# Performance work log

Measured on AMD Instinct MI355X. Metric: run time of the kernel, lower is better.

## Reference

```python
import jax, jax.numpy as jnp
import numpy as np

DIM = 768
NUM_HEADS = 12
HEAD_DIM = DIM // NUM_HEADS
SCALE = HEAD_DIM ** -0.5


def setup_inputs() -> dict:
    key = jax.random.key(0)
    k1, k2, k3, k4 = jax.random.split(key, 4)
    B, N, C = 4, 2048, DIM
    x = jax.random.normal(k1, (B, N, C), dtype=jnp.float32)
    # nn.Linear(dim, 3*dim, bias=False): weight shape (3C, C), y = x @ W^T
    w_qkv = jax.random.normal(k2, (3 * C, C), dtype=jnp.float32) * (C ** -0.5)
    # nn.Linear(dim, dim) with default bias=True
    w_proj = jax.random.normal(k3, (C, C), dtype=jnp.float32) * (C ** -0.5)
    b_proj = jax.random.normal(k4, (C,), dtype=jnp.float32) * 0.02
    return {"x": x, "w_qkv": w_qkv, "w_proj": w_proj, "b_proj": b_proj}


def reference(x, w_qkv, w_proj, b_proj):
    B, N, C = x.shape
    H, D = NUM_HEADS, HEAD_DIM
    qkv = jnp.einsum('bnc,oc->bno', x, w_qkv)  # (B, N, 3C)
    qkv = qkv.reshape(B, N, 3, H, D).transpose(2, 0, 3, 1, 4)  # (3, B, H, N, D)
    q, k, v = qkv[0], qkv[1], qkv[2]
    attn = jnp.einsum('bhnd,bhmd->bhnm', q, k) * jnp.float32(SCALE)  # (B,H,N,N)
    attn = jax.nn.softmax(attn, axis=-1)
    out = jnp.einsum('bhnm,bhmd->bhnd', attn, v)  # (B,H,N,D)
    out = out.transpose(0, 2, 1, 3).reshape(B, N, C)
    out = jnp.einsum('bnc,oc->bno', out, w_proj) + b_proj
    return out
```

## Files before the change

kernel.cpp:

```cpp
#include <hip/hip_runtime.h>
#include <math.h>

#define B_ 4
#define N_ 2048
#define C_ 768
#define H_ 12
#define D_ 64
#define QKSCALE_ 0.18033688011112042f

typedef unsigned short u16;
typedef unsigned int u32;
typedef short s16x8 __attribute__((ext_vector_type(8)));
typedef float f32x4 __attribute__((ext_vector_type(4)));
typedef float f32x16 __attribute__((ext_vector_type(16)));

__device__ __forceinline__ u16 f2bf(float f) {
    union { float f; u32 u; } v; v.f = f;
    u32 r = (v.u + 0x7fffu + ((v.u >> 16) & 1u)) >> 16;
    return (u16)r;
}

__device__ __forceinline__ void gl_lds16(const u16* g, u16* l) {
    __builtin_amdgcn_global_load_lds(
        (__attribute__((address_space(1))) void*)g,
        (__attribute__((address_space(3))) void*)l, 16, 0, 0);
}

#define NX4_  (B_ * N_ * C_ / 4)
#define NWQ4_ (3 * C_ * C_ / 4)
#define NWP4_ (C_ * C_ / 4)
__global__ __launch_bounds__(256) void cvt_all(const float4* __restrict__ x,
                                               const float4* __restrict__ wq,
                                               const float4* __restrict__ wp,
                                               ushort4* __restrict__ xb,
                                               ushort4* __restrict__ wqb,
                                               ushort4* __restrict__ wpb)
{
    const int tot = NX4_ + NWQ4_ + NWP4_;
    int i = blockIdx.x * blockDim.x + threadIdx.x;
    const int stride = gridDim.x * blockDim.x;
    for (; i < tot; i += stride) {
        const float4* s; ushort4* d; int j;
        if (i < NX4_)              { s = x;  d = xb;  j = i; }
        else if (i < NX4_ + NWQ4_) { s = wq; d = wqb; j = i - NX4_; }
        else                       { s = wp; d = wpb; j = i - NX4_ - NWQ4_; }
        float4 v = s[j];
        ushort4 o;
        o.x = f2bf(v.x); o.y = f2bf(v.y); o.z = f2bf(v.z); o.w = f2bf(v.w);
        d[j] = o;
    }
}

template<int BM, int WPEU, bool OUT_BF16, bool BIAS, bool QSCALE>
__global__ __launch_bounds__(256, WPEU) void gemm_mfma(const u16* __restrict__ A,
                                                       const u16* __restrict__ Bm,
                                                       const float* __restrict__ bias,
                                                       void* __restrict__ Cout,
                                                       int M, int N, int K)
{
    constexpr int MF  = BM / 32;
    constexpr int AC  = BM / 32;
    constexpr int ASZ = BM * 64, BSZ = 128 * 64;
    __shared__ __align__(16) u16 As[2 * ASZ];
    __shared__ __align__(16) u16 Bs[2 * BSZ];
    const int tid  = threadIdx.x;
    const int wv   = tid >> 6;
    const int lane = tid & 63;
    const int lr   = lane & 15;
    const int lq   = lane >> 4;
    const int wm   = (wv >> 1) * (BM / 2);
    const int wn   = (wv & 1) * 64;
    const int row0 = blockIdx.y * BM, col0 = blockIdx.x * 128;

    f32x4 acc[MF][4];
    #pragma unroll
    for (int i = 0; i < MF; i++)
        #pragma unroll
        for (int j = 0; j < 4; j++) { f32x4 z = {0.f,0.f,0.f,0.f}; acc[i][j] = z; }

    const int srow   = lane >> 3;
    const int schunk = ((lane & 7) ^ srow) * 8;

    const int arow_base = (BM / 4) * wv;
    const u16* gA = A + (size_t)(row0 + arow_base + srow) * K + schunk;
    const u16* gB = Bm + (size_t)(col0 + 32 * wv + srow) * K + schunk;
    const int aoff = arow_base * 64;
    const int boff = (32 * wv) * 64;

    const int nIter = K / 64;

    #pragma unroll
    for (int c = 0; c < AC; c++)
        gl_lds16(gA + (size_t)(8 * c) * K, As + aoff + c * 8 * 64);
    #pragma unroll
    for (int c = 0; c < 4; c++)
        gl_lds16(gB + (size_t)(8 * c) * K, Bs + boff + c * 8 * 64);

    for (int t = 0; t < nIter; t++) {
        const int cur = t & 1;
        __syncthreads();
        if (t + 1 < nIter) {
            const int k1 = (t + 1) * 64;
            const int nb = cur ^ 1;
            #pragma unroll
            for (int c = 0; c < AC; c++)
                gl_lds16(gA + (size_t)(8 * c) * K + k1, As + nb * ASZ + aoff + c * 8 * 64);
            #pragma unroll
            for (int c = 0; c < 4; c++)
                gl_lds16(gB + (size_t)(8 * c) * K + k1, Bs + nb * BSZ + boff + c * 8 * 64);
        }
        const u16* __restrict__ Ac = As + cur * ASZ;
        const u16* __restrict__ Bc = Bs + cur * BSZ;
        #pragma unroll
        for (int kk = 0; kk < 2; kk++) {
            const int fo = ((4 * kk + lq) ^ (lr & 7)) * 8;
            s16x8 af[MF], bfr[4];
            #pragma unroll
            for (int i = 0; i < MF; i++)
                af[i] = *(const s16x8*)&Ac[(wm + 16*i + lr) * 64 + fo];
            #pragma unroll
            for (int j = 0; j < 4; j++)
                bfr[j] = *(const s16x8*)&Bc[(wn + 16*j + lr) * 64 + fo];
            #pragma unroll
            for (int i = 0; i < MF; i++)
                #pragma unroll
                for (int j = 0; j < 4; j++)
                    acc[i][j] = __builtin_amdgcn_mfma_f32_16x16x32_bf16(af[i], bfr[j], acc[i][j], 0, 0, 0);
        }
    }

    #pragma unroll
    for (int i = 0; i < MF; i++) {
        #pragma unroll
        for (int j = 0; j < 4; j++) {
            const int col = col0 + wn + 16*j + lr;
            float bv = BIAS ? bias[col] : 0.f;
            #pragma unroll
            for (int r = 0; r < 4; r++) {
                const int row = row0 + wm + 16*i + lq*4 + r;
                float v = acc[i][j][r] + bv;
                if (QSCALE && col < C_) v *= QKSCALE_;
                if (OUT_BF16) ((u16*)Cout)[(size_t)row * N + col] = f2bf(v);
                else          ((float*)Cout)[(size_t)row * N + col] = v;
            }
        }
    }
}

__global__ __launch_bounds__(256, 3) void attn_mfma(const u16* __restrict__ qkv,
                                                    u16* __restrict__ attout)
{
    __shared__ __align__(16) u16 Ks[2][64 * 64];
    __shared__ __align__(16) u16 Vt[2][64][72];

    const int tid  = threadIdx.x;
    const int wv   = tid >> 6;
    const int lane = tid & 63;
    const int l31  = lane & 31;
    const int hi   = lane >> 5;

    const int wgid = blockIdx.y * gridDim.x + blockIdx.x;
    const int ix   = wgid >> 3;
    const int bh   = (wgid & 7) * 6 + (ix >> 4);
    const int n0   = (ix & 15) * 128;
    const int b = bh / H_, h = bh % H_;
    const size_t rs = 3 * C_;

    const u16* Qg = qkv + ((size_t)b * N_ + n0) * rs + h * D_;
    const u16* Kg = qkv + ((size_t)b * N_) * rs + C_ + h * D_;
    const u16* Vg = Kg + C_;

    s16x8 qf[4];
    #pragma unroll
    for (int kk = 0; kk < 4; kk++)
        qf[kk] = *(const s16x8*)(Qg + (size_t)(32*wv + l31) * rs + kk*16 + hi*8);

    const f32x16 z16 = {0.f,0.f,0.f,0.f,0.f,0.f,0.f,0.f,
                        0.f,0.f,0.f,0.f,0.f,0.f,0.f,0.f};
    f32x16 oacc[2] = {z16, z16};
    float li = 0.f;

    const int kkey = lane >> 3;
    const u16* Kg_l = Kg + (size_t)(16*wv + kkey) * rs + ((lane & 7) ^ kkey) * 8;

    const int vc = tid & 7, vp = tid >> 3;
    const int vkey0 = 2 * vp, vd0 = vc * 8;
    const int vcol0 = (vkey0 + 8 * vc) & 63;

    gl_lds16(Kg_l,                    &Ks[0][(16*wv) * 64]);
    gl_lds16(Kg_l + (size_t)8 * rs,   &Ks[0][(16*wv + 8) * 64]);

    s16x8 vr0, vr1;
    {
        const u16* vp2 = Vg + (size_t)vkey0 * rs + vd0;
        vr0 = *(const s16x8*)vp2; vr1 = *(const s16x8*)(vp2 + rs);
    }
    #pragma unroll
    for (int u = 0; u < 8; u++) {
        u32 pk = (u32)(u16)vr0[u] | ((u32)(u16)vr1[u] << 16);
        *(u32*)&Vt[0][vd0 + u][vcol0] = pk;
    }
    {
        const u16* vp2 = Vg + (size_t)(64 + vkey0) * rs + vd0;
        vr0 = *(const s16x8*)vp2; vr1 = *(const s16x8*)(vp2 + rs);
    }

    const int NT = N_ / 64;
    for (int t = 0; t < NT; t++) {
        const int cur = t & 1, nxt = cur ^ 1;
        __syncthreads();
        if (t + 1 < NT) {
            const size_t ko = (size_t)(t + 1) * 64 * rs;
            gl_lds16(Kg_l + ko,                  &Ks[nxt][(16*wv) * 64]);
            gl_lds16(Kg_l + ko + (size_t)8 * rs, &Ks[nxt][(16*wv + 8) * 64]);
            #pragma unroll
            for (int u = 0; u < 8; u++) {
                u32 pk = (u32)(u16)vr0[u] | ((u32)(u16)vr1[u] << 16);
                *(u32*)&Vt[nxt][vd0 + u][vcol0] = pk;
            }
        }
        if (t + 2 < NT) {
            const u16* vp2 = Vg + (size_t)((t+2)*64 + vkey0) * rs + vd0;
            vr0 = *(const s16x8*)vp2; vr1 = *(const s16x8*)(vp2 + rs);
        }

        #define KF(j, kk) (*(const s16x8*)&Ks[cur][(32*(j) + l31) * 64 + \
                           ((2*(kk) + hi) ^ (l31 & 7)) * 8])
        f32x16 st0 = __builtin_amdgcn_mfma_f32_32x32x16_bf16(KF(0,0), qf[0], z16, 0, 0, 0);
        f32x16 st1 = __builtin_amdgcn_mfma_f32_32x32x16_bf16(KF(1,0), qf[0], z16, 0, 0, 0);
        #pragma unroll
        for (int kk = 1; kk < 4; kk++) {
            st0 = __builtin_amdgcn_mfma_f32_32x32x16_bf16(KF(0,kk), qf[kk], st0, 0, 0, 0);
            st1 = __builtin_amdgcn_mfma_f32_32x32x16_bf16(KF(1,kk), qf[kk], st1, 0, 0, 0);
        }
        #undef KF

        #pragma unroll
        for (int j = 0; j < 2; j++) {
            const f32x16 s = j ? st1 : st0;
            float p[16];
            #pragma unroll
            for (int r = 0; r < 16; r++) p[r] = __builtin_amdgcn_exp2f(s[r]);
            #pragma unroll
            for (int r = 0; r < 16; r += 4)
                li += (p[r] + p[r+1]) + (p[r+2] + p[r+3]);
            u32 w[4][2];
            #pragma unroll
            for (int m = 0; m < 4; m++) {
                asm("v_cvt_pk_bf16_f32 %0, %1, %2"
                    : "=v"(w[m][0]) : "v"(p[4*m+0]), "v"(p[4*m+1]));
                asm("v_cvt_pk_bf16_f32 %0, %1, %2"
                    : "=v"(w[m][1]) : "v"(p[4*m+2]), "v"(p[4*m+3]));
            }
            #pragma unroll
            for (int h2 = 0; h2 < 2; h2++) {
                asm("v_permlane32_swap_b32 %0, %1"
                    : "+v"(w[2*h2][0]), "+v"(w[2*h2+1][0]));
                asm("v_permlane32_swap_b32 %0, %1"
                    : "+v"(w[2*h2][1]), "+v"(w[2*h2+1][1]));
                const int sp = 2*j + h2;
                union { u32 uw[4]; s16x8 v; } pa;
                pa.uw[0] = w[2*h2][0];   pa.uw[1] = w[2*h2][1];
                pa.uw[2] = w[2*h2+1][0]; pa.uw[3] = w[2*h2+1][1];
                #pragma unroll
                for (int j2 = 0; j2 < 2; j2++) {
                    const int pb = (2*sp + hi + 4*j2 + (l31 >> 3)) & 7;
                    s16x8 vb = *(const s16x8*)&Vt[cur][32*j2 + l31][pb * 8];
                    oacc[j2] = __builtin_amdgcn_mfma_f32_32x32x16_bf16(pa.v, vb, oacc[j2], 0, 0, 0);
                }
            }
        }
    }

    li += __shfl_xor(li, 32);
    const float inv = 1.f / li;
    #pragma unroll
    for (int r = 0; r < 16; r++) {
        const int qr = (r & 3) + 8 * (r >> 2) + 4 * hi;
        const float iv = __shfl(inv, qr);
        const size_t grow = (size_t)(b * N_ + n0 + 32*wv + qr);
        #pragma unroll
        for (int j2 = 0; j2 < 2; j2++)
            attout[grow * C_ + h * D_ + 32*j2 + l31] = f2bf(oacc[j2][r] * iv);
    }
}

extern "C" void kernel_launch(void* const* d_in, const int* in_sizes, int n_in,
                              void* d_out, int out_size, void* d_ws, size_t ws_size,
                              hipStream_t stream) {
    const float* x      = (const float*)d_in[0];
    const float* w_qkv  = (const float*)d_in[1];
    const float* w_proj = (const float*)d_in[2];
    const float* b_proj = (const float*)d_in[3];
    float* out = (float*)d_out;

    const int NX   = B_ * N_ * C_;
    const int NWQ  = 3 * C_ * C_;
    const int NWP  = C_ * C_;
    const int NQKV = B_ * N_ * 3 * C_;

    u16* xb   = (u16*)d_ws;
    u16* wqb  = xb + NX;
    u16* wpb  = wqb + NWQ;
    u16* qkvb = wpb + NWP;
    u16* attb = qkvb + NQKV;

    dim3 blk(256);

    cvt_all<<<768, blk, 0, stream>>>((const float4*)x, (const float4*)w_qkv,
                                     (const float4*)w_proj,
                                     (ushort4*)xb, (ushort4*)wqb, (ushort4*)wpb);

    const int M = B_ * N_;
    gemm_mfma<128, 2, true, false, true><<<dim3((3*C_)/128, M/128), blk, 0, stream>>>(
        xb, wqb, nullptr, qkvb, M, 3*C_, C_);

    attn_mfma<<<dim3(N_/128, B_ * H_), blk, 0, stream>>>(qkvb, attb);

    gemm_mfma<64, 3, false, true, false><<<dim3(C_/128, M/64), blk, 0, stream>>>(
        attb, wpb, b_proj, out, M, C_, C_);
}
```

Baseline: 212.2 us.

## Process two 32-row query tiles per wave in attention, halving block threads

The attention kernel now runs 2 waves (128 threads) per block instead of 4, and each wave handles 64 query rows as two 32-row tiles. Each K fragment read from LDS and each V fragment feeds two MFMAs instead of one, which halves LDS read traffic per unit of compute. The cooperative K/V staging now has each thread load twice as much. In exchange the kernel needs more registers per wave (two sets of accumulators, Q fragments and softmax sums), and each block has fewer waves to hide latency, which may lower occupancy.

```diff
diff --git a/kernel.cpp b/kernel.cpp
--- a/kernel.cpp
+++ b/kernel.cpp
@@ -147,7 +147,7 @@
     }
 }
 
-__global__ __launch_bounds__(256, 3) void attn_mfma(const u16* __restrict__ qkv,
+__global__ __launch_bounds__(128, 2) void attn_mfma(const u16* __restrict__ qkv,
                                                     u16* __restrict__ attout)
 {
     __shared__ __align__(16) u16 Ks[2][64 * 64];
@@ -170,40 +170,48 @@
     const u16* Kg = qkv + ((size_t)b * N_) * rs + C_ + h * D_;
     const u16* Vg = Kg + C_;
 
-    s16x8 qf[4];
-    #pragma unroll
-    for (int kk = 0; kk < 4; kk++)
-        qf[kk] = *(const s16x8*)(Qg + (size_t)(32*wv + l31) * rs + kk*16 + hi*8);
+    s16x8 qf[2][4];
+    #pragma unroll
+    for (int q = 0; q < 2; q++)
+        #pragma unroll
+        for (int kk = 0; kk < 4; kk++)
+            qf[q][kk] = *(const s16x8*)(Qg + (size_t)(64*wv + 32*q + l31) * rs + kk*16 + hi*8);
 
     const f32x16 z16 = {0.f,0.f,0.f,0.f,0.f,0.f,0.f,0.f,
                         0.f,0.f,0.f,0.f,0.f,0.f,0.f,0.f};
-    f32x16 oacc[2] = {z16, z16};
-    float li = 0.f;
+    f32x16 oacc[2][2] = {{z16, z16}, {z16, z16}};
+    float li[2] = {0.f, 0.f};
 
     const int kkey = lane >> 3;
-    const u16* Kg_l = Kg + (size_t)(16*wv + kkey) * rs + ((lane & 7) ^ kkey) * 8;
+    const u16* Kg_l = Kg + (size_t)(32*wv + kkey) * rs + ((lane & 7) ^ kkey) * 8;
 
     const int vc = tid & 7, vp = tid >> 3;
-    const int vkey0 = 2 * vp, vd0 = vc * 8;
-    const int vcol0 = (vkey0 + 8 * vc) & 63;
-
-    gl_lds16(Kg_l,                    &Ks[0][(16*wv) * 64]);
-    gl_lds16(Kg_l + (size_t)8 * rs,   &Ks[0][(16*wv + 8) * 64]);
-
-    s16x8 vr0, vr1;
-    {
-        const u16* vp2 = Vg + (size_t)vkey0 * rs + vd0;
-        vr0 = *(const s16x8*)vp2; vr1 = *(const s16x8*)(vp2 + rs);
-    }
-    #pragma unroll
-    for (int u = 0; u < 8; u++) {
-        u32 pk = (u32)(u16)vr0[u] | ((u32)(u16)vr1[u] << 16);
-        *(u32*)&Vt[0][vd0 + u][vcol0] = pk;
-    }
-    {
-        const u16* vp2 = Vg + (size_t)(64 + vkey0) * rs + vd0;
-        vr0 = *(const s16x8*)vp2; vr1 = *(const s16x8*)(vp2 + rs);
-    }
+    const int vkey0 = 4 * vp, vd0 = vc * 8;
+    const int col01 = (vkey0     + vd0) & 63;
+    const int col23 = (vkey0 + 2 + vd0) & 63;
+
+    s16x8 vr[4];
+    #define VLOAD(t) do { \
+        const u16* vp2 = Vg + ((size_t)(t)*64 + vkey0) * rs + vd0; \
+        vr[0] = *(const s16x8*)vp2;            vr[1] = *(const s16x8*)(vp2 + rs); \
+        vr[2] = *(const s16x8*)(vp2 + 2*rs);   vr[3] = *(const s16x8*)(vp2 + 3*rs); \
+    } while (0)
+    #define VWRITE(slot) do { \
+        _Pragma("unroll") \
+        for (int u = 0; u < 8; u++) { \
+            u32 pkA = (u32)(u16)vr[0][u] | ((u32)(u16)vr[1][u] << 16); \
+            u32 pkB = (u32)(u16)vr[2][u] | ((u32)(u16)vr[3][u] << 16); \
+            *(u32*)&Vt[slot][vd0 + u][col01] = pkA; \
+            *(u32*)&Vt[slot][vd0 + u][col23] = pkB; \
+        } \
+    } while (0)
+
+    #pragma unroll
+    for (int c = 0; c < 4; c++)
+        gl_lds16(Kg_l + (size_t)(8*c) * rs, &Ks[0][(32*wv + 8*c) * 64]);
+    VLOAD(0);
+    VWRITE(0);
+    VLOAD(1);
 
     const int NT = N_ / 64;
     for (int t = 0; t < NT; t++) {
@@ -211,78 +219,99 @@
         __syncthreads();
         if (t + 1 < NT) {
             const size_t ko = (size_t)(t + 1) * 64 * rs;
-            gl_lds16(Kg_l + ko,                  &Ks[nxt][(16*wv) * 64]);
-            gl_lds16(Kg_l + ko + (size_t)8 * rs, &Ks[nxt][(16*wv + 8) * 64]);
-            #pragma unroll
-            for (int u = 0; u < 8; u++) {
-                u32 pk = (u32)(u16)vr0[u] | ((u32)(u16)vr1[u] << 16);
-                *(u32*)&Vt[nxt][vd0 + u][vcol0] = pk;
-            }
-        }
-        if (t + 2 < NT) {
-            const u16* vp2 = Vg + (size_t)((t+2)*64 + vkey0) * rs + vd0;
-            vr0 = *(const s16x8*)vp2; vr1 = *(const s16x8*)(vp2 + rs);
-        }
+            #pragma unroll
+            for (int c = 0; c < 4; c++)
+                gl_lds16(Kg_l + ko + (size_t)(8*c) * rs, &Ks[nxt][(32*wv + 8*c) * 64]);
+            VWRITE(nxt);
+        }
+        if (t + 2 < NT)
+            VLOAD(t + 2);
 
         #define KF(j, kk) (*(const s16x8*)&Ks[cur][(32*(j) + l31) * 64 + \
                            ((2*(kk) + hi) ^ (l31 & 7)) * 8])
-        f32x16 st0 = __builtin_amdgcn_mfma_f32_32x32x16_bf16(KF(0,0), qf[0], z16, 0, 0, 0);
-        f32x16 st1 = __builtin_amdgcn_mfma_f32_32x32x16_bf16(KF(1,0), qf[0], z16, 0, 0, 0);
-        #pragma unroll
-        for (int kk = 1; kk < 4; kk++) {
-            st0 = __builtin_amdgcn_mfma_f32_32x32x16_bf16(KF(0,kk), qf[kk], st0, 0, 0, 0);
-            st1 = __builtin_amdgcn_mfma_f32_32x32x16_bf16(KF(1,kk), qf[kk], st1, 0, 0, 0);
-        }
+        f32x16 st[2][2];
+        #pragma unroll
+        for (int j = 0; j < 2; j++) {
+            s16x8 kf = KF(j, 0);
+            st[0][j] = __builtin_amdgcn_mfma_f32_32x32x16_bf16(kf, qf[0][0], z16, 0, 0, 0);
+            st[1][j] = __builtin_amdgcn_mfma_f32_32x32x16_bf16(kf, qf[1][0], z16, 0, 0, 0);
+        }
+        #pragma unroll
+        for (int kk = 1; kk < 4; kk++)
+            #pragma unroll
+            for (int j = 0; j < 2; j++) {
+                s16x8 kf = KF(j, kk);
+                st[0][j] = __builtin_amdgcn_mfma_f32_32x32x16_bf16(kf, qf[0][kk], st[0][j], 0, 0, 0);
+                st[1][j] = __builtin_amdgcn_mfma_f32_32x32x16_bf16(kf, qf[1][kk], st[1][j], 0, 0, 0);
+            }
         #undef KF
 
         #pragma unroll
         for (int j = 0; j < 2; j++) {
-            const f32x16 s = j ? st1 : st0;
-            float p[16];
-            #pragma unroll
-            for (int r = 0; r < 16; r++) p[r] = __builtin_amdgcn_exp2f(s[r]);
-            #pragma unroll
-            for (int r = 0; r < 16; r += 4)
-                li += (p[r] + p[r+1]) + (p[r+2] + p[r+3]);
-            u32 w[4][2];
-            #pragma unroll
-            for (int m = 0; m < 4; m++) {
-                asm("v_cvt_pk_bf16_f32 %0, %1, %2"
-                    : "=v"(w[m][0]) : "v"(p[4*m+0]), "v"(p[4*m+1]));
-                asm("v_cvt_pk_bf16_f32 %0, %1, %2"
-                    : "=v"(w[m][1]) : "v"(p[4*m+2]), "v"(p[4*m+3]));
+            u32 paw[2][2][4];
+            #pragma unroll
+            for (int q = 0; q < 2; q++) {
+                const f32x16 s = st[q][j];
+                float p[16];
+                #pragma unroll
+                for (int r = 0; r < 16; r++) p[r] = __builtin_amdgcn_exp2f(s[r]);
+                #pragma unroll
+                for (int r = 0; r < 16; r += 4)
+                    li[q] += (p[r] + p[r+1]) + (p[r+2] + p[r+3]);
+                u32 w[4][2];
+                #pragma unroll
+                for (int m = 0; m < 4; m++) {
+                    asm("v_cvt_pk_bf16_f32 %0, %1, %2"
+                        : "=v"(w[m][0]) : "v"(p[4*m+0]), "v"(p[4*m+1]));
+                    asm("v_cvt_pk_bf16_f32 %0, %1, %2"
+                        : "=v"(w[m][1]) : "v"(p[4*m+2]), "v"(p[4*m+3]));
+                }
+                #pragma unroll
+                for (int h2 = 0; h2 < 2; h2++) {
+                    asm("v_permlane32_swap_b32 %0, %1"
+                        : "+v"(w[2*h2][0]), "+v"(w[2*h2+1][0]));
+                    asm("v_permlane32_swap_b32 %0, %1"
+                        : "+v"(w[2*h2][1]), "+v"(w[2*h2+1][1]));
+                    paw[q][h2][0] = w[2*h2][0];   paw[q][h2][1] = w[2*h2][1];
+                    paw[q][h2][2] = w[2*h2+1][0]; paw[q][h2][3] = w[2*h2+1][1];
+                }
             }
             #pragma unroll
             for (int h2 = 0; h2 < 2; h2++) {
-                asm("v_permlane32_swap_b32 %0, %1"
-                    : "+v"(w[2*h2][0]), "+v"(w[2*h2+1][0]));
-                asm("v_permlane32_swap_b32 %0, %1"
-                    : "+v"(w[2*h2][1]), "+v"(w[2*h2+1][1]));
                 const int sp = 2*j + h2;
-                union { u32 uw[4]; s16x8 v; } pa;
-                pa.uw[0] = w[2*h2][0];   pa.uw[1] = w[2*h2][1];
-                pa.uw[2] = w[2*h2+1][0]; pa.uw[3] = w[2*h2+1][1];
+                union { u32 uw[4]; s16x8 v; } pa0, pa1;
+                pa0.uw[0] = paw[0][h2][0]; pa0.uw[1] = paw[0][h2][1];
+                pa0.uw[2] = paw[0][h2][2]; pa0.uw[3] = paw[0][h2][3];
+                pa1.uw[0] = paw[1][h2][0]; pa1.uw[1] = paw[1][h2][1];
+                pa1.uw[2] = paw[1][h2][2]; pa1.uw[3] = paw[1][h2][3];
                 #pragma unroll
                 for (int j2 = 0; j2 < 2; j2++) {
                     const int pb = (2*sp + hi + 4*j2 + (l31 >> 3)) & 7;
                     s16x8 vb = *(const s16x8*)&Vt[cur][32*j2 + l31][pb * 8];
-                    oacc[j2] = __builtin_amdgcn_mfma_f32_32x32x16_bf16(pa.v, vb, oacc[j2], 0, 0, 0);
+                    oacc[0][j2] = __builtin_amdgcn_mfma_f32_32x32x16_bf16(pa0.v, vb, oacc[0][j2], 0, 0, 0);
+                    oacc[1][j2] = __builtin_amdgcn_mfma_f32_32x32x16_bf16(pa1.v, vb, oacc[1][j2], 0, 0, 0);
                 }
             }
         }
     }
 
-    li += __shfl_xor(li, 32);
-    const float inv = 1.f / li;
-    #pragma unroll
-    for (int r = 0; r < 16; r++) {
-        const int qr = (r & 3) + 8 * (r >> 2) + 4 * hi;
-        const float iv = __shfl(inv, qr);
-        const size_t grow = (size_t)(b * N_ + n0 + 32*wv + qr);
-        #pragma unroll
-        for (int j2 = 0; j2 < 2; j2++)
-            attout[grow * C_ + h * D_ + 32*j2 + l31] = f2bf(oacc[j2][r] * iv);
-    }
+    #pragma unroll
+    for (int q = 0; q < 2; q++) {
+        float lq = li[q];
+        lq += __shfl_xor(lq, 32);
+        const float inv = 1.f / lq;
+        #pragma unroll
+        for (int r = 0; r < 16; r++) {
+            const int qr = (r & 3) + 8 * (r >> 2) + 4 * hi;
+            const float iv = __shfl(inv, qr);
+            const size_t grow = (size_t)(b * N_ + n0 + 64*wv + 32*q + qr);
+            #pragma unroll
+            for (int j2 = 0; j2 < 2; j2++)
+                attout[grow * C_ + h * D_ + 32*j2 + l31] = f2bf(oacc[q][j2][r] * iv);
+        }
+    }
+    #undef VLOAD
+    #undef VWRITE
 }
 
 extern "C" void kernel_launch(void* const* d_in, const int* in_sizes, int n_in,
@@ -315,7 +344,7 @@
     gemm_mfma<128, 2, true, false, true><<<dim3((3*C_)/128, M/128), blk, 0, stream>>>(
         xb, wqb, nullptr, qkvb, M, 3*C_, C_);
 
-    attn_mfma<<<dim3(N_/128, B_ * H_), blk, 0, stream>>>(qkvb, attb);
+    attn_mfma<<<dim3(N_/128, B_ * H_), dim3(128), 0, stream>>>(qkvb, attb);
 
     gemm_mfma<64, 3, false, true, false><<<dim3(C_/128, M/64), blk, 0, stream>>>(
         attb, wpb, b_proj, out, M, C_, C_);
```

Result: slower. 217.5 us (+2.5%).
